# Kernel tuning notes

Hardware: AMD Instinct MI355X
Metric: run time of the kernel (lower is better)

Reference implementation:

```python
import jax, jax.numpy as jnp
import numpy as np

B, T, W_DIM = 32, 2048, 1024
G, D = 16, 64          # num_groups, input_dim (w = G*D)
MOM = 0.9
TH = 0.5
EPS = 1e-8
TOP_K = 2


def setup_inputs() -> dict:
    key = jax.random.key(0)
    k = jax.random.split(key, 4)
    x = jax.random.normal(k[0], (B, T, W_DIM), dtype=jnp.float32)
    ema = jnp.zeros((W_DIM, W_DIM), dtype=jnp.float32)
    W1 = jax.random.normal(k[1], (G, 16, D), dtype=jnp.float32) * 0.05
    b1 = jnp.zeros((G, 16), dtype=jnp.float32)
    W2 = jax.random.normal(k[2], (G, 1, 16), dtype=jnp.float32) * 0.05
    b2 = jnp.zeros((G, 1), dtype=jnp.float32)
    return {"x": x, "ema": ema, "W1": W1, "b1": b1, "W2": W2, "b2": b2}


def _corr_over_T(x):
    # x: (B, T, w) -> per-batch Pearson corr over the T axis: (B, w, w)
    Tn = x.shape[1]
    c = x - x.mean(axis=1, keepdims=True)
    cov = jnp.einsum('btw,btv->bwv', c, c) / (Tn - 1)
    std = jnp.sqrt(jnp.sum(c * c, axis=1) / (Tn - 1))  # (B, w)
    return jnp.clip(cov / (std[:, :, None] * std[:, None, :] + EPS), -1.0, 1.0)


def reference(x, ema, W1, b1, W2, b2):
    # --- burst-masked EMA update (torch.no_grad) ---
    corr_batch = jax.lax.stop_gradient(_corr_over_T(x))  # (B, w, w)

    def step(e, c):
        mask = jnp.abs(c) > TH
        return jnp.where(mask, MOM * e + (1.0 - MOM) * c, e), None

    ema_new, _ = jax.lax.scan(step, ema, corr_batch)

    # --- split into groups: (B, T, G, D) ---
    Bn, Tn, w = x.shape
    groups = x.reshape(Bn, Tn, G, D)

    # --- per-group correlation score: mean |off-diagonal| of within-group corr ---
    cg = groups - groups.mean(axis=1, keepdims=True)
    cov_g = jnp.einsum('btgd,btge->bgde', cg, cg) / (Tn - 1)        # (B, G, D, D)
    std_g = jnp.sqrt(jnp.sum(cg * cg, axis=1) / (Tn - 1))           # (B, G, D)
    corr_g = jnp.clip(cov_g / (std_g[..., :, None] * std_g[..., None, :] + EPS), -1.0, 1.0)
    absc = jnp.abs(corr_g)
    offdiag = (absc.sum(axis=(-2, -1)) - jnp.einsum('bgdd->bg', absc)) / (D * D - D)
    correlations = offdiag.mean(axis=0)                              # (G,)

    # --- select the 2 least-correlated groups (these get gradients) ---
    _, sel = jax.lax.top_k(-correlations, TOP_K)
    sel_mask = jnp.zeros((G,), dtype=bool).at[sel].set(True)

    # --- per-group expert MLP: D -> 16 -> 1, batched over groups ---
    h = jax.nn.relu(jnp.einsum('btgd,ghd->btgh', groups, W1) + b1)   # (B, T, G, 16)
    o = (jnp.einsum('btgh,goh->btgo', h, W2) + b2)[..., 0]           # (B, T, G)

    # non-selected groups run under no_grad -> stop_gradient on their outputs
    out = jnp.where(sel_mask[None, None, :], o, jax.lax.stop_gradient(o))
    return out, correlations, ema_new
```

## Files before the change

kernel.cpp:

```cpp
#include <hip/hip_runtime.h>
#include <hip/hip_bf16.h>
#include <stdint.h>

#define B_   32
#define T_   2048
#define W_   1024
#define G_   16
#define D_   64
#define LIST_CAP 65536
#define BK   64

typedef __bf16 bf16_t;
typedef __bf16 bf16x8 __attribute__((ext_vector_type(8)));
typedef float  f32x4  __attribute__((ext_vector_type(4)));

#define WS_XT      0ull
#define WS_XT_SZ   (134217728ull)
#define WS_SUM     (WS_XT + WS_XT_SZ)
#define WS_SQ      (WS_SUM + 131072ull)
#define WS_MU      (WS_SQ  + 131072ull)
#define WS_SIG     (WS_MU  + 131072ull)
#define WS_ACCUM   (WS_SIG + 131072ull)
#define WS_LISTCNT (WS_ACCUM + 256ull)
#define WS_LIST    (WS_LISTCNT + 256ull)
#define WS_MASK    (WS_LIST + 1048576ull)
#define WS_DIAG    (WS_MASK + 4194304ull)

__global__ __launch_bounds__(256) void stats_transpose(
    const float* __restrict__ x, bf16_t* __restrict__ xT,
    float* __restrict__ sumb, float* __restrict__ sqb) {
  int b = blockIdx.z, t0 = blockIdx.x * 64, w0 = blockIdx.y * 64;
  __shared__ float tile[64][65];
  __shared__ float rs[64][17], rq[64][17];
  int tid = threadIdx.x;
  int wc = tid & 15, tr = tid >> 4;
  float4 s4 = {0.f, 0.f, 0.f, 0.f}, q4 = {0.f, 0.f, 0.f, 0.f};
  const float4* xp = (const float4*)(x + ((size_t)b * T_ + t0) * W_ + w0);
#pragma unroll
  for (int p = 0; p < 4; ++p) {
    int t = tr + 16 * p;
    float4 v = xp[(size_t)t * 256 + wc];
    s4.x += v.x; s4.y += v.y; s4.z += v.z; s4.w += v.w;
    q4.x += v.x * v.x; q4.y += v.y * v.y; q4.z += v.z * v.z; q4.w += v.w * v.w;
    tile[4 * wc + 0][t] = v.x;
    tile[4 * wc + 1][t] = v.y;
    tile[4 * wc + 2][t] = v.z;
    tile[4 * wc + 3][t] = v.w;
  }
  rs[4 * wc + 0][tr] = s4.x; rs[4 * wc + 1][tr] = s4.y;
  rs[4 * wc + 2][tr] = s4.z; rs[4 * wc + 3][tr] = s4.w;
  rq[4 * wc + 0][tr] = q4.x; rq[4 * wc + 1][tr] = q4.y;
  rq[4 * wc + 2][tr] = q4.z; rq[4 * wc + 3][tr] = q4.w;
  __syncthreads();
  if (tid < 64) {
    float s = 0.f, q = 0.f;
#pragma unroll
    for (int i = 0; i < 16; ++i) { s += rs[tid][i]; q += rq[tid][i]; }
    atomicAdd(&sumb[b * W_ + w0 + tid], s);
    atomicAdd(&sqb[b * W_ + w0 + tid], q);
  }
  int c = tid & 7, wv = tid >> 3;
#pragma unroll
  for (int p = 0; p < 2; ++p) {
    int w = wv + 32 * p;
    const float* src = &tile[w][c * 8];
    bf16x8 o;
#pragma unroll
    for (int k = 0; k < 8; ++k) o[k] = (bf16_t)src[k];
    *(bf16x8*)(xT + ((size_t)b * W_ + w0 + w) * T_ + t0 + c * 8) = o;
  }
}

__global__ void finalize_stats(const float* __restrict__ sumb,
                               const float* __restrict__ sqb,
                               float* __restrict__ mu, float* __restrict__ sig) {
  int idx = blockIdx.x * 256 + threadIdx.x;
  float s = sumb[idx], q = sqb[idx];
  float m = s * (1.0f / 2048.0f);
  float var = (q - s * m) * (1.0f / 2047.0f);
  if (var < 0.f) var = 0.f;
  mu[idx] = m;
  sig[idx] = sqrtf(var);
}

__global__ __launch_bounds__(256) void gram_kernel(
    const bf16_t* __restrict__ xT, const float* __restrict__ mu,
    const float* __restrict__ sig, unsigned int* __restrict__ mask,
    float* __restrict__ diagv, int* __restrict__ listcnt,
    int4* __restrict__ list, float* __restrict__ accum) {
  int id = blockIdx.x;
  int xcd = id & 7;
  int idx = id >> 3;
  int sub = idx / 36;
  int rt  = idx % 36;
  int b = sub * 8 + xcd;
  int r = rt, ti = 0;
  while (r >= 8 - ti) { r -= 8 - ti; ++ti; }
  int tj = ti + r;
  int i0 = ti * 128, j0 = tj * 128;

  const bf16_t* Ag = xT + ((size_t)b * W_ + i0) * T_;
  const bf16_t* Bg = xT + ((size_t)b * W_ + j0) * T_;

  __shared__ __attribute__((aligned(16))) bf16_t As[128 * BK];
  __shared__ __attribute__((aligned(16))) bf16_t Bs[128 * BK];

  int tid = threadIdx.x;
  int lane = tid & 63, wave = tid >> 6;
  int wm = wave >> 1, wn = wave & 1;

  f32x4 zero = {0.f, 0.f, 0.f, 0.f};
  f32x4 acc[4][4];
#pragma unroll
  for (int mi = 0; mi < 4; ++mi)
#pragma unroll
    for (int nj = 0; nj < 4; ++nj) acc[mi][nj] = zero;

  int arow = wm * 64 + (lane & 15);
  int brow = wn * 64 + (lane & 15);
  int q = lane >> 4;

  for (int k0 = 0; k0 < T_; k0 += BK) {
    __syncthreads();
#pragma unroll
    for (int s = 0; s < 4; ++s) {
      int c = s * 256 + tid;
      int row = c >> 3, slot = c & 7;
      int gslot = slot ^ (row & 7);
      __builtin_amdgcn_global_load_lds(
          (const __attribute__((address_space(1))) void*)(Ag + (size_t)row * T_ + k0 + gslot * 8),
          (__attribute__((address_space(3))) void*)(As + c * 8), 16, 0, 0);
      __builtin_amdgcn_global_load_lds(
          (const __attribute__((address_space(1))) void*)(Bg + (size_t)row * T_ + k0 + gslot * 8),
          (__attribute__((address_space(3))) void*)(Bs + c * 8), 16, 0, 0);
    }
    __syncthreads();

#pragma unroll
    for (int s2 = 0; s2 < 2; ++s2) {
      bf16x8 af[4], bfr[4];
#pragma unroll
      for (int mi = 0; mi < 4; ++mi) {
        int row = arow + mi * 16;
        af[mi] = *(const bf16x8*)(As + row * BK + ((s2 * 4 + q) ^ (row & 7)) * 8);
      }
#pragma unroll
      for (int nj = 0; nj < 4; ++nj) {
        int row = brow + nj * 16;
        bfr[nj] = *(const bf16x8*)(Bs + row * BK + ((s2 * 4 + q) ^ (row & 7)) * 8);
      }
#pragma unroll
      for (int mi = 0; mi < 4; ++mi)
#pragma unroll
        for (int nj = 0; nj < 4; ++nj)
          acc[mi][nj] = __builtin_amdgcn_mfma_f32_16x16x32_bf16(af[mi], bfr[nj], acc[mi][nj], 0, 0, 0);
    }
  }

  const float inv = 1.0f / 2047.0f;
  const float* mub = mu + b * W_;
  const float* sgb = sig + b * W_;
  bool diagquad = (ti == tj) && (wm == wn);
  float gsum = 0.f;

#pragma unroll
  for (int nj = 0; nj < 4; ++nj) {
    int j = j0 + wn * 64 + nj * 16 + (lane & 15);
    float muj = mub[j], sgj = sgb[j];
#pragma unroll
    for (int mi = 0; mi < 4; ++mi) {
#pragma unroll
      for (int rr = 0; rr < 4; ++rr) {
        int i = i0 + wm * 64 + mi * 16 + (lane >> 4) * 4 + rr;
        float cov = (acc[mi][nj][rr] - 2048.0f * mub[i] * muj) * inv;
        float corr = cov / (sgb[i] * sgj + 1e-8f);
        corr = fminf(1.0f, fmaxf(-1.0f, corr));
        if (diagquad && (i != j)) gsum += fabsf(corr);
        if (fabsf(corr) > 0.5f) {
          atomicOr(&mask[i * W_ + j], 1u << b);
          if (i == j) {
            diagv[b * W_ + i] = corr;
          } else {
            int p = atomicAdd(listcnt, 1);
            if (p < LIST_CAP) list[p] = make_int4(b, i, j, __float_as_int(corr));
          }
          if (ti != tj) {
            atomicOr(&mask[j * W_ + i], 1u << b);
            int p = atomicAdd(listcnt, 1);
            if (p < LIST_CAP) list[p] = make_int4(b, j, i, __float_as_int(corr));
          }
        }
      }
    }
  }
  if (diagquad) {
    for (int o = 32; o > 0; o >>= 1) gsum += __shfl_down(gsum, o);
    if (lane == 0) atomicAdd(&accum[ti * 2 + wm], gsum);
  }
}

__global__ void ema_kernel(const float* __restrict__ ema,
                           const unsigned int* __restrict__ mask,
                           const float* __restrict__ diagv,
                           const int* __restrict__ listcnt,
                           const int4* __restrict__ list,
                           float* __restrict__ emaout) {
  int idx = blockIdx.x * 256 + threadIdx.x;
  int i = idx >> 10, j = idx & 1023;
  float e = ema[idx];
  unsigned int m = mask[idx];
  if (m) {
    if (i == j) {
      for (int b = 0; b < 32; ++b)
        if ((m >> b) & 1u) e = 0.9f * e + 0.1f * diagv[b * W_ + i];
    } else {
      int cnt = *listcnt; if (cnt > LIST_CAP) cnt = LIST_CAP;
      for (int b = 0; b < 32; ++b) {
        if ((m >> b) & 1u) {
          for (int k = 0; k < cnt; ++k) {
            int4 t = list[k];
            if (t.x == b && t.y == i && t.z == j) {
              e = 0.9f * e + 0.1f * __int_as_float(t.w);
              break;
            }
          }
        }
      }
    }
  }
  emaout[idx] = e;
}

__global__ void corr_finalize(const float* __restrict__ accum, float* __restrict__ outc) {
  int g = threadIdx.x;
  if (g < 16) outc[g] = accum[g] * (1.0f / (32.0f * 4032.0f));
}

__global__ __launch_bounds__(256) void mlp_kernel(
    const float* __restrict__ x, const float* __restrict__ W1,
    const float* __restrict__ b1, const float* __restrict__ W2,
    const float* __restrict__ b2, float* __restrict__ out) {
  int b = blockIdx.y, t0 = blockIdx.x * 64, gs = blockIdx.z * 4;
  int tid = threadIdx.x;
  int gl = tid & 3, tl = tid >> 2;
  __shared__ float Wt[16 * 64 * 4];
  __shared__ float b1s[16 * 4], W2s[16 * 4], b2s[4];
  for (int l = tid; l < 4096; l += 256) {
    int g2 = l & 3, jd = l >> 2;
    Wt[l] = W1[(size_t)(gs + g2) * 1024 + jd];
  }
  if (tid < 64) {
    int g2 = tid & 3, j = tid >> 2;
    b1s[j * 4 + g2] = b1[(gs + g2) * 16 + j];
    W2s[j * 4 + g2] = W2[(gs + g2) * 16 + j];
  }
  if (tid < 4) b2s[tid] = b2[gs + tid];
  __syncthreads();

  int g = gs + gl, t = t0 + tl;
  const float4* xp = (const float4*)(x + ((size_t)b * T_ + t) * W_ + g * D_);
  float h[16];
#pragma unroll
  for (int j = 0; j < 16; ++j) h[j] = b1s[j * 4 + gl];
#pragma unroll
  for (int d4 = 0; d4 < 16; ++d4) {
    float4 xv = xp[d4];
#pragma unroll
    for (int j = 0; j < 16; ++j) {
      const float* wp = &Wt[(j * 64 + d4 * 4) * 4 + gl];
      h[j] += xv.x * wp[0] + xv.y * wp[4] + xv.z * wp[8] + xv.w * wp[12];
    }
  }
  float o = b2s[gl];
#pragma unroll
  for (int j = 0; j < 16; ++j) o += fmaxf(h[j], 0.f) * W2s[j * 4 + gl];
  out[((size_t)b * T_ + t) * 16 + g] = o;
}

extern "C" void kernel_launch(void* const* d_in, const int* in_sizes, int n_in,
                              void* d_out, int out_size, void* d_ws, size_t ws_size,
                              hipStream_t stream) {
  const float* x   = (const float*)d_in[0];
  const float* ema = (const float*)d_in[1];
  const float* W1  = (const float*)d_in[2];
  const float* b1  = (const float*)d_in[3];
  const float* W2  = (const float*)d_in[4];
  const float* b2  = (const float*)d_in[5];

  float* out    = (float*)d_out;
  float* outc   = out + 1048576;
  float* outema = outc + 16;

  char* ws = (char*)d_ws;
  bf16_t* xT        = (bf16_t*)(ws + WS_XT);
  float* sumb       = (float*)(ws + WS_SUM);
  float* sqb        = (float*)(ws + WS_SQ);
  float* mub        = (float*)(ws + WS_MU);
  float* sigb       = (float*)(ws + WS_SIG);
  float* accum      = (float*)(ws + WS_ACCUM);
  int*   listcnt    = (int*)(ws + WS_LISTCNT);
  int4*  list       = (int4*)(ws + WS_LIST);
  unsigned int* msk = (unsigned int*)(ws + WS_MASK);
  float* diagv      = (float*)(ws + WS_DIAG);

  hipMemsetAsync(ws + WS_SUM, 0, 262144, stream);
  hipMemsetAsync(ws + WS_ACCUM, 0, 512, stream);
  hipMemsetAsync(ws + WS_MASK, 0, 4194304, stream);

  stats_transpose<<<dim3(32, 16, 32), 256, 0, stream>>>(x, xT, sumb, sqb);
  finalize_stats<<<128, 256, 0, stream>>>(sumb, sqb, mub, sigb);
  gram_kernel<<<1152, 256, 0, stream>>>(xT, mub, sigb, msk, diagv, listcnt, list, accum);
  ema_kernel<<<4096, 256, 0, stream>>>(ema, msk, diagv, listcnt, list, outema);
  corr_finalize<<<1, 16, 0, stream>>>(accum, outc);
  mlp_kernel<<<dim3(32, 32, 4), 256, 0, stream>>>(x, W1, b1, W2, b2, out);
}
```

Baseline: 728.0 us.

## Double-buffer correlation GEMM LDS tiles and vectorize MLP weight reads

The bf16 correlation GEMM now uses two LDS buffers. The next K tile is issued through global_load_lds while the current one is consumed, with explicit vmcnt waits and barriers replacing the load-then-sync pattern. The MLP kernel's weight table is re-laid out per group with a padded row stride, so each thread reads float4 vectors instead of four strided scalar LDS reads. This doubles LDS use in the GEMM, which may reduce occupancy, and relies on the hand-written vmcnt count matching the number of outstanding loads.

```diff
diff --git a/kernel.cpp b/kernel.cpp
--- a/kernel.cpp
+++ b/kernel.cpp
@@ -102,26 +102,16 @@
   const bf16_t* Ag = xT + ((size_t)b * W_ + i0) * T_;
   const bf16_t* Bg = xT + ((size_t)b * W_ + j0) * T_;
 
-  __shared__ __attribute__((aligned(16))) bf16_t As[128 * BK];
-  __shared__ __attribute__((aligned(16))) bf16_t Bs[128 * BK];
+  __shared__ __attribute__((aligned(16))) bf16_t As[2][128 * BK];
+  __shared__ __attribute__((aligned(16))) bf16_t Bs[2][128 * BK];
 
   int tid = threadIdx.x;
   int lane = tid & 63, wave = tid >> 6;
   int wm = wave >> 1, wn = wave & 1;
 
-  f32x4 zero = {0.f, 0.f, 0.f, 0.f};
-  f32x4 acc[4][4];
-#pragma unroll
-  for (int mi = 0; mi < 4; ++mi)
-#pragma unroll
-    for (int nj = 0; nj < 4; ++nj) acc[mi][nj] = zero;
-
-  int arow = wm * 64 + (lane & 15);
-  int brow = wn * 64 + (lane & 15);
-  int q = lane >> 4;
-
-  for (int k0 = 0; k0 < T_; k0 += BK) {
-    __syncthreads();
+  auto stage = [&](int buf, int k0) {
+    bf16_t* Ad = &As[buf][0];
+    bf16_t* Bd = &Bs[buf][0];
 #pragma unroll
     for (int s = 0; s < 4; ++s) {
       int c = s * 256 + tid;
@@ -129,25 +119,53 @@
       int gslot = slot ^ (row & 7);
       __builtin_amdgcn_global_load_lds(
           (const __attribute__((address_space(1))) void*)(Ag + (size_t)row * T_ + k0 + gslot * 8),
-          (__attribute__((address_space(3))) void*)(As + c * 8), 16, 0, 0);
+          (__attribute__((address_space(3))) void*)(Ad + c * 8), 16, 0, 0);
       __builtin_amdgcn_global_load_lds(
           (const __attribute__((address_space(1))) void*)(Bg + (size_t)row * T_ + k0 + gslot * 8),
-          (__attribute__((address_space(3))) void*)(Bs + c * 8), 16, 0, 0);
-    }
-    __syncthreads();
-
+          (__attribute__((address_space(3))) void*)(Bd + c * 8), 16, 0, 0);
+    }
+  };
+
+  f32x4 zero = {0.f, 0.f, 0.f, 0.f};
+  f32x4 acc[4][4];
+#pragma unroll
+  for (int mi = 0; mi < 4; ++mi)
+#pragma unroll
+    for (int nj = 0; nj < 4; ++nj) acc[mi][nj] = zero;
+
+  int arow = wm * 64 + (lane & 15);
+  int brow = wn * 64 + (lane & 15);
+  int q = lane >> 4;
+
+  stage(0, 0);
+
+  const int NT = T_ / BK;
+#pragma unroll 1
+  for (int kt = 0; kt < NT; ++kt) {
+    int cur = kt & 1;
+    if (kt + 1 < NT) {
+      stage(cur ^ 1, (kt + 1) * BK);
+      asm volatile("s_waitcnt vmcnt(8)" ::: "memory");
+    } else {
+      asm volatile("s_waitcnt vmcnt(0)" ::: "memory");
+    }
+    __builtin_amdgcn_s_barrier();
+    __builtin_amdgcn_sched_barrier(0);
+
+    const bf16_t* Ac = &As[cur][0];
+    const bf16_t* Bc = &Bs[cur][0];
 #pragma unroll
     for (int s2 = 0; s2 < 2; ++s2) {
       bf16x8 af[4], bfr[4];
 #pragma unroll
       for (int mi = 0; mi < 4; ++mi) {
         int row = arow + mi * 16;
-        af[mi] = *(const bf16x8*)(As + row * BK + ((s2 * 4 + q) ^ (row & 7)) * 8);
+        af[mi] = *(const bf16x8*)(Ac + row * BK + ((s2 * 4 + q) ^ (row & 7)) * 8);
       }
 #pragma unroll
       for (int nj = 0; nj < 4; ++nj) {
         int row = brow + nj * 16;
-        bfr[nj] = *(const bf16x8*)(Bs + row * BK + ((s2 * 4 + q) ^ (row & 7)) * 8);
+        bfr[nj] = *(const bf16x8*)(Bc + row * BK + ((s2 * 4 + q) ^ (row & 7)) * 8);
       }
 #pragma unroll
       for (int mi = 0; mi < 4; ++mi)
@@ -155,6 +173,9 @@
         for (int nj = 0; nj < 4; ++nj)
           acc[mi][nj] = __builtin_amdgcn_mfma_f32_16x16x32_bf16(af[mi], bfr[nj], acc[mi][nj], 0, 0, 0);
     }
+    asm volatile("s_waitcnt lgkmcnt(0)" ::: "memory");
+    __builtin_amdgcn_sched_barrier(0);
+    __builtin_amdgcn_s_barrier();
   }
 
   const float inv = 1.0f / 2047.0f;
@@ -243,11 +264,12 @@
   int b = blockIdx.y, t0 = blockIdx.x * 64, gs = blockIdx.z * 4;
   int tid = threadIdx.x;
   int gl = tid & 3, tl = tid >> 2;
-  __shared__ float Wt[16 * 64 * 4];
+  __shared__ __attribute__((aligned(16))) float Wt[4 * 1092 + 16];
   __shared__ float b1s[16 * 4], W2s[16 * 4], b2s[4];
   for (int l = tid; l < 4096; l += 256) {
-    int g2 = l & 3, jd = l >> 2;
-    Wt[l] = W1[(size_t)(gs + g2) * 1024 + jd];
+    int g2 = l >> 10, r = l & 1023;
+    int j = r >> 6, d = r & 63;
+    Wt[g2 * 1092 + j * 68 + d] = W1[(size_t)(gs + g2) * 1024 + r];
   }
   if (tid < 64) {
     int g2 = tid & 3, j = tid >> 2;
@@ -259,6 +281,7 @@
 
   int g = gs + gl, t = t0 + tl;
   const float4* xp = (const float4*)(x + ((size_t)b * T_ + t) * W_ + g * D_);
+  const float* wbase = &Wt[gl * 1092];
   float h[16];
 #pragma unroll
   for (int j = 0; j < 16; ++j) h[j] = b1s[j * 4 + gl];
@@ -267,8 +290,8 @@
     float4 xv = xp[d4];
 #pragma unroll
     for (int j = 0; j < 16; ++j) {
-      const float* wp = &Wt[(j * 64 + d4 * 4) * 4 + gl];
-      h[j] += xv.x * wp[0] + xv.y * wp[4] + xv.z * wp[8] + xv.w * wp[12];
+      float4 wv = *(const float4*)(wbase + j * 68 + d4 * 4);
+      h[j] += xv.x * wv.x + xv.y * wv.y + xv.z * wv.z + xv.w * wv.w;
     }
   }
   float o = b2s[gl];
```

After: 698.7 us. 1.04x faster.
